# Optimization experiments

Measured on AMD Instinct MI355X. Metric: run time of the kernel, lower is better.

## Reference

```python
import jax, jax.numpy as jnp
import numpy as np
import math

B, T, D, H = 4, 1024, 1024, 16
DK = D // H
TAU_THRESH = 0.3


def setup_inputs() -> dict:
    key = jax.random.key(0)
    ks = jax.random.split(key, 13)
    s = 1.0 / math.sqrt(D)
    return {
        "x": jax.random.normal(ks[0], (B, T, D), dtype=jnp.float32),
        "Wq": jax.random.normal(ks[1], (D, D), dtype=jnp.float32) * s,
        "bq": jax.random.normal(ks[2], (D,), dtype=jnp.float32) * s,
        "Wk": jax.random.normal(ks[3], (D, D), dtype=jnp.float32) * s,
        "bk": jax.random.normal(ks[4], (D,), dtype=jnp.float32) * s,
        "Wv": jax.random.normal(ks[5], (D, D), dtype=jnp.float32) * s,
        "bv": jax.random.normal(ks[6], (D,), dtype=jnp.float32) * s,
        "Wo": jax.random.normal(ks[7], (D, D), dtype=jnp.float32) * s,
        "bo": jax.random.normal(ks[8], (D,), dtype=jnp.float32) * s,
        "Wg1": jax.random.normal(ks[9], (1, D), dtype=jnp.float32) * s,
        "bg1": jax.random.normal(ks[10], (1,), dtype=jnp.float32) * s,
        "Wg2": jax.random.normal(ks[11], (1, D), dtype=jnp.float32) * s,
        "bg2": jax.random.normal(ks[12], (1,), dtype=jnp.float32) * s,
    }


def reference(x, Wq, bq, Wk, bk, Wv, bv, Wo, bo, Wg1, bg1, Wg2, bg2):
    b, t, d = x.shape
    # projections (torch Linear: y = x @ W.T + b)
    Q = (x @ Wq.T + bq).reshape(b, t, H, DK).transpose(0, 2, 1, 3)  # [B,H,T,dk]
    K = (x @ Wk.T + bk).reshape(b, t, H, DK).transpose(0, 2, 1, 3)
    V = (x @ Wv.T + bv).reshape(b, t, H, DK).transpose(0, 2, 1, 3)
    scores = jnp.einsum("bhqd,bhkd->bhqk", Q, K) / math.sqrt(DK)  # [B,H,T,T]
    # confidence gates from first-token query context [B, H*dk] = [B, D]
    context = Q[:, :, 0, :].reshape(b, d)
    q1 = jax.nn.sigmoid(context @ Wg1.T + bg1)  # [B,1]
    q2 = jax.nn.sigmoid(context @ Wg2.T + bg2)  # [B,1]
    c = jnp.clip(q1 * q2, 1e-8, 1.0)            # [B,1]
    tau = jnp.where(c < TAU_THRESH, 1.0 / c, jnp.ones_like(c)).reshape(b, 1, 1, 1)
    p = jax.nn.softmax(scores / tau, axis=-1)
    cb = c.reshape(b, 1, 1, 1)
    p_gated = cb * p + (1.0 - cb) * (1.0 / t)
    u = jnp.mean(1.0 - c, axis=-1, keepdims=True)  # [B,1]
    attn_out = jnp.einsum("bhqk,bhkd->bhqd", p_gated, V)
    attn_out = attn_out.transpose(0, 2, 1, 3).reshape(b, t, d)
    output = attn_out @ Wo.T + bo
    return output, u
```

## Files before the change

kernel.cpp:

```cpp
#include <hip/hip_runtime.h>
#include <stdint.h>

typedef short bf16x8 __attribute__((ext_vector_type(8)));
typedef float f32x4 __attribute__((ext_vector_type(4)));

#define MFMA_BF16(a, b, c) __builtin_amdgcn_mfma_f32_16x16x32_bf16((a), (b), (c), 0, 0, 0)

__device__ __forceinline__ short f2bf(float x) {
  union { float f; uint32_t u; } v; v.f = x;
  uint32_t r = (v.u + 0x7FFFu + ((v.u >> 16) & 1u)) >> 16;
  return (short)r;
}
__device__ __forceinline__ uint32_t rnd_bf_hi(float x) {
  union { float f; uint32_t u; } v; v.f = x;
  return v.u + 0x7FFFu + ((v.u >> 16) & 1u);
}
__device__ __forceinline__ uint32_t pack2bf(float a, float b) {
  return __builtin_amdgcn_perm(rnd_bf_hi(b), rnd_bf_hi(a), 0x07060302);
}
__device__ __forceinline__ float bfbits2f(uint32_t b16) {
  union { uint32_t u; float f; } v; v.u = b16 << 16; return v.f;
}
__device__ __forceinline__ float fexp2(float x) {
#if __has_builtin(__builtin_amdgcn_exp2f)
  return __builtin_amdgcn_exp2f(x);
#else
  return __expf(x * 0.6931471805599453f);
#endif
}
__device__ __forceinline__ void async16(const void* g, void* l) {
  __builtin_amdgcn_global_load_lds(
      (const __attribute__((address_space(1))) uint32_t*)g,
      (__attribute__((address_space(3))) uint32_t*)l, 16, 0, 0);
}

__global__ __launch_bounds__(256) void prep_k(
    const float* __restrict__ x, const float* __restrict__ Wq,
    const float* __restrict__ Wk, const float* __restrict__ Wv,
    const float* __restrict__ Wo, const float* __restrict__ bq,
    short* __restrict__ xb, short* __restrict__ Wqb, short* __restrict__ Wkb,
    short* __restrict__ Wvb, short* __restrict__ Wob, float* __restrict__ ctx) {
  __shared__ float xs[1024];
  const int bid = blockIdx.x;
  const int tid = threadIdx.x;
  if (bid < 8192) {
    const float* src; short* dst; int idx;
    if (bid < 4096) {
      src = x; dst = xb; idx = (bid << 8) + tid;
    } else {
      const int r = bid - 4096;
      const int z = r >> 10;
      src = (z == 0) ? Wq : (z == 1) ? Wk : (z == 2) ? Wv : Wo;
      dst = (z == 0) ? Wqb : (z == 1) ? Wkb : (z == 2) ? Wvb : Wob;
      idx = ((r & 1023) << 8) + tid;
    }
    float4 v = ((const float4*)src)[idx];
    short4 o;
    o.x = f2bf(v.x); o.y = f2bf(v.y); o.z = f2bf(v.z); o.w = f2bf(v.w);
    ((short4*)dst)[idx] = o;
  } else {
    const int r = bid - 8192;
    const int b = r >> 4;
    const int n0 = (r & 15) << 6;
    for (int i = tid; i < 1024; i += 256) xs[i] = x[b * 1048576 + i];
    __syncthreads();
    const int w = tid >> 6, lane = tid & 63;
    const float4* xv4 = (const float4*)xs;
    for (int rr = 0; rr < 16; ++rr) {
      const int n = n0 + (w << 4) + rr;
      const float4* wrow = (const float4*)(Wq + n * 1024);
      float p = 0.f;
#pragma unroll
      for (int c2 = 0; c2 < 4; ++c2) {
        float4 wv = wrow[lane + (c2 << 6)];
        float4 xv = xv4[lane + (c2 << 6)];
        p += xv.x * wv.x + xv.y * wv.y + xv.z * wv.z + xv.w * wv.w;
      }
#pragma unroll
      for (int off = 32; off; off >>= 1) p += __shfl_xor(p, off);
      if (lane == 0) ctx[b * 1024 + n] = p + bq[n];
    }
  }
}

__global__ __launch_bounds__(256) void gates_fin(const float* __restrict__ ctx,
                                                 const float* __restrict__ Wg1,
                                                 const float* __restrict__ bg1,
                                                 const float* __restrict__ Wg2,
                                                 const float* __restrict__ bg2,
                                                 float* __restrict__ gates,
                                                 float* __restrict__ u_out) {
  __shared__ float red[16];
  const int tid = threadIdx.x, w = tid >> 6, lane = tid & 63;
  for (int b = 0; b < 4; ++b) {
    float4 cv = ((const float4*)(ctx + b * 1024))[tid];
    float4 w1 = ((const float4*)Wg1)[tid];
    float4 w2 = ((const float4*)Wg2)[tid];
    float p1 = cv.x * w1.x + cv.y * w1.y + cv.z * w1.z + cv.w * w1.w;
    float p2 = cv.x * w2.x + cv.y * w2.y + cv.z * w2.z + cv.w * w2.w;
#pragma unroll
    for (int off = 32; off; off >>= 1) { p1 += __shfl_xor(p1, off); p2 += __shfl_xor(p2, off); }
    if (lane == 0) { red[w] = p1; red[8 + w] = p2; }
    __syncthreads();
    if (tid == 0) {
      float g1 = red[0] + red[1] + red[2] + red[3] + bg1[0];
      float g2 = red[8] + red[9] + red[10] + red[11] + bg2[0];
      float q1 = 1.f / (1.f + expf(-g1));
      float q2 = 1.f / (1.f + expf(-g2));
      float c = fminf(fmaxf(q1 * q2, 1e-8f), 1.0f);
      gates[b * 2 + 0] = c;
      gates[b * 2 + 1] = (c < 0.3f ? c : 1.0f) * 0.125f * 1.4426950408889634f;
      u_out[b] = 1.0f - c;
    }
    __syncthreads();
  }
}

template <bool SWP>
__device__ __forceinline__ void qkv_core128(
    const short* __restrict__ A, const short* __restrict__ W,
    const float* __restrict__ bias, short* __restrict__ out,
    short* As, short* Bs, int m0, int n0) {
  const int tid = threadIdx.x;
  const int w = tid >> 6, lane = tid & 63;
  const int m15 = lane & 15, quad = lane >> 4;
  const int wr = w >> 1, wc = w & 1;

  f32x4 acc[4][4];
#pragma unroll
  for (int i = 0; i < 4; ++i)
#pragma unroll
    for (int j = 0; j < 4; ++j) { f32x4 zz = {0.f, 0.f, 0.f, 0.f}; acc[i][j] = zz; }

  const int srow = (w << 5) + (lane >> 2);
  const int sxor = (srow >> 1) & 3;
  const int scol = (((lane & 3) ^ sxor) << 3);
  const short* ga0 = A + (m0 + srow) * 1024 + scol;
  const short* ga1 = ga0 + 16 * 1024;
  const short* gb0 = W + (n0 + srow) * 1024 + scol;
  const short* gb1 = gb0 + 16 * 1024;
  short* la0 = &As[srow * 32 + ((lane & 3) << 3)];
  short* la1 = la0 + 512;
  short* lb0 = &Bs[srow * 32 + ((lane & 3) << 3)];
  short* lb1 = lb0 + 512;

  for (int kt = 0; kt < 32; ++kt) {
    async16(ga0, la0); async16(ga1, la1);
    async16(gb0, lb0); async16(gb1, lb1);
    ga0 += 32; ga1 += 32; gb0 += 32; gb1 += 32;
    __syncthreads();
    bf16x8 a[4], b[4];
#pragma unroll
    for (int i = 0; i < 4; ++i) {
      const int ra = (wr << 6) + (i << 4) + m15;
      a[i] = *(const bf16x8*)(&As[ra * 32 + ((quad ^ ((ra >> 1) & 3)) << 3)]);
    }
#pragma unroll
    for (int j = 0; j < 4; ++j) {
      const int rb = (wc << 6) + (j << 4) + m15;
      b[j] = *(const bf16x8*)(&Bs[rb * 32 + ((quad ^ ((rb >> 1) & 3)) << 3)]);
    }
#pragma unroll
    for (int i = 0; i < 4; ++i)
#pragma unroll
      for (int j = 0; j < 4; ++j) {
        if (SWP) acc[i][j] = MFMA_BF16(b[j], a[i], acc[i][j]);
        else     acc[i][j] = MFMA_BF16(a[i], b[j], acc[i][j]);
      }
    __syncthreads();
  }

  if (SWP) {
#pragma unroll
    for (int j = 0; j < 4; ++j) {
      const int n = n0 + (wc << 6) + (j << 4) + (quad << 2);
      const float4 bv = *(const float4*)(bias + n);
      const int hh = n >> 6, dk0 = n & 63;
#pragma unroll
      for (int i = 0; i < 4; ++i) {
        const int m = m0 + (wr << 6) + (i << 4) + m15;
        const int bb = m >> 10, tt = m & 1023;
        uint2 st;
        st.x = pack2bf(acc[i][j][0] + bv.x, acc[i][j][1] + bv.y);
        st.y = pack2bf(acc[i][j][2] + bv.z, acc[i][j][3] + bv.w);
        *(uint2*)(out + (((bb << 4) + hh) << 16) + (tt << 6) + dk0) = st;
      }
    }
  } else {
#pragma unroll
    for (int j = 0; j < 4; ++j) {
      const int n = n0 + (wc << 6) + (j << 4) + m15;
      const float bv = bias[n];
      const int hh = n >> 6, dk = n & 63;
#pragma unroll
      for (int i = 0; i < 4; ++i) {
        const int m = m0 + (wr << 6) + (i << 4) + (quad << 2);
        const int bb = m >> 10, t0 = m & 1023;
        uint2 st;
        st.x = pack2bf(acc[i][j][0] + bv, acc[i][j][1] + bv);
        st.y = pack2bf(acc[i][j][2] + bv, acc[i][j][3] + bv);
        *(uint2*)(out + (((bb << 4) + hh) << 16) + (dk << 10) + t0) = st;
      }
    }
  }
}

__global__ __launch_bounds__(256) void gemm_qkv(
    const short* __restrict__ xb,
    const short* __restrict__ Wqb, const short* __restrict__ Wkb, const short* __restrict__ Wvb,
    const float* __restrict__ bq, const float* __restrict__ bk, const float* __restrict__ bv,
    short* __restrict__ Qh, short* __restrict__ Kh, short* __restrict__ Vt) {
  __shared__ short As[4096];
  __shared__ short Bs[4096];
  const int z = blockIdx.z;
  const int m0 = blockIdx.x << 7, n0 = blockIdx.y << 7;
  if (z == 0)      qkv_core128<true >(xb, Wqb, bq, Qh, As, Bs, m0, n0);
  else if (z == 1) qkv_core128<true >(xb, Wkb, bk, Kh, As, Bs, m0, n0);
  else             qkv_core128<false>(xb, Wvb, bv, Vt, As, Bs, m0, n0);
}

__global__ __launch_bounds__(256) void gemm_out(const short* __restrict__ Ab,
                                                const short* __restrict__ Wo,
                                                const float* __restrict__ bo,
                                                float* __restrict__ Cout) {
  const int m0 = blockIdx.x << 7;
  const int n0 = blockIdx.y << 7;
  const int tid = threadIdx.x;
  const int w = tid >> 6, lane = tid & 63;
  const int m15 = lane & 15, quad = lane >> 4;
  const int wr = w >> 1, wc = w & 1;

  __shared__ short As[4096];
  __shared__ short Bs[4096];

  f32x4 acc[4][4];
#pragma unroll
  for (int i = 0; i < 4; ++i)
#pragma unroll
    for (int j = 0; j < 4; ++j) { f32x4 zz = {0.f, 0.f, 0.f, 0.f}; acc[i][j] = zz; }

  const int srow = (w << 5) + (lane >> 2);
  const int sxor = (srow >> 1) & 3;
  const int scol = (((lane & 3) ^ sxor) << 3);
  const short* ga0 = Ab + (m0 + srow) * 1024 + scol;
  const short* ga1 = ga0 + 16 * 1024;
  const short* gb0 = Wo + (n0 + srow) * 1024 + scol;
  const short* gb1 = gb0 + 16 * 1024;
  short* la0 = &As[srow * 32 + ((lane & 3) << 3)];
  short* la1 = la0 + 512;
  short* lb0 = &Bs[srow * 32 + ((lane & 3) << 3)];
  short* lb1 = lb0 + 512;

  for (int kt = 0; kt < 32; ++kt) {
    async16(ga0, la0); async16(ga1, la1);
    async16(gb0, lb0); async16(gb1, lb1);
    ga0 += 32; ga1 += 32; gb0 += 32; gb1 += 32;
    __syncthreads();
    bf16x8 a[4], b[4];
#pragma unroll
    for (int i = 0; i < 4; ++i) {
      const int ra = (wr << 6) + (i << 4) + m15;
      a[i] = *(const bf16x8*)(&As[ra * 32 + ((quad ^ ((ra >> 1) & 3)) << 3)]);
    }
#pragma unroll
    for (int j = 0; j < 4; ++j) {
      const int rb = (wc << 6) + (j << 4) + m15;
      b[j] = *(const bf16x8*)(&Bs[rb * 32 + ((quad ^ ((rb >> 1) & 3)) << 3)]);
    }
#pragma unroll
    for (int i = 0; i < 4; ++i)
#pragma unroll
      for (int j = 0; j < 4; ++j)
        acc[i][j] = MFMA_BF16(a[i], b[j], acc[i][j]);
    __syncthreads();
  }

#pragma unroll
  for (int j = 0; j < 4; ++j) {
    const int n = n0 + (wc << 6) + (j << 4) + m15;
    const float bb_ = bo[n];
#pragma unroll
    for (int i = 0; i < 4; ++i) {
      const int mb = m0 + (wr << 6) + (i << 4) + (quad << 2);
#pragma unroll
      for (int r = 0; r < 4; ++r)
        Cout[(mb + r) * 1024 + n] = acc[i][j][r] + bb_;
    }
  }
}

__global__ __launch_bounds__(256, 2) void attn_k(const short* __restrict__ Qh,
                                                 const short* __restrict__ Kh,
                                                 const short* __restrict__ Vt,
                                                 const float* __restrict__ gates,
                                                 short* __restrict__ attnb) {
  const int bh = blockIdx.x;
  const int b = bh >> 4, h = bh & 15;
  const int q0 = blockIdx.y << 7;
  const int tid = threadIdx.x;
  const int w = tid >> 6, lane = tid & 63;
  const int m15 = lane & 15, quad = lane >> 4;

  __shared__ short Ks[2][4096];
  __shared__ short Vs[3][4096];

  const short* ksrc = Kh + bh * 65536;
  const short* vsrc = Vt + bh * 65536;

  const float sl = gates[b * 2 + 1];

  const short* qsrcA = Qh + ((bh << 10) + q0 + (w << 4) + m15) * 64;
  const short* qsrcB = qsrcA + 64 * 64;
  const bf16x8 qA0 = *(const bf16x8*)(qsrcA + (quad << 3));
  const bf16x8 qA1 = *(const bf16x8*)(qsrcA + 32 + (quad << 3));
  const bf16x8 qB0 = *(const bf16x8*)(qsrcB + (quad << 3));
  const bf16x8 qB1 = *(const bf16x8*)(qsrcB + 32 + (quad << 3));

  const bf16x8 vone = {0x3F80, 0x3F80, 0x3F80, 0x3F80, 0x3F80, 0x3F80, 0x3F80, 0x3F80};

  const int off0 = tid, off1 = tid + 256;
  const int r0 = off0 >> 3, cb0 = (off0 & 7) ^ (r0 & 7);
  const int r1 = off1 >> 3, cb1 = (off1 & 7) ^ (r1 & 7);

#define STAGE(kv, kb, vb)                                                      \
  do {                                                                         \
    async16(ksrc + (((kv) << 6) + r0) * 64 + (cb0 << 3), &Ks[kb][off0 << 3]);  \
    async16(ksrc + (((kv) << 6) + r1) * 64 + (cb1 << 3), &Ks[kb][off1 << 3]);  \
    async16(vsrc + r0 * 1024 + ((kv) << 6) + (cb0 << 3), &Vs[vb][off0 << 3]);  \
    async16(vsrc + r1 * 1024 + ((kv) << 6) + (cb1 << 3), &Vs[vb][off1 << 3]);  \
  } while (0)

  STAGE(0, 0, 0);

  float lsumA = 0.f, lsumB = 0.f;
  f32x4 oA[4], oB[4], o_mv[4];
#pragma unroll
  for (int jd = 0; jd < 4; ++jd) {
    f32x4 zz = {0.f, 0.f, 0.f, 0.f};
    oA[jd] = zz; oB[jd] = zz; o_mv[jd] = zz;
  }

  const int srcA = ((quad & 1) << 5) + m15;
  const int srcB = srcA + 16;
  const bool selhi = (quad & 2) != 0;

#define BUILD_PF(pf, pk)                                                       \
  do {                                                                         \
    _Pragma("unroll")                                                          \
    for (int Hh = 0; Hh < 2; ++Hh) {                                           \
      uint32_t f[4];                                                           \
      _Pragma("unroll")                                                        \
      for (int rp = 0; rp < 2; ++rp) {                                         \
        uint32_t alo = (uint32_t)__shfl((int)pk[2 * Hh][rp], srcA);            \
        uint32_t ahi = (uint32_t)__shfl((int)pk[2 * Hh + 1][rp], srcA);        \
        uint32_t blo = (uint32_t)__shfl((int)pk[2 * Hh][rp], srcB);            \
        uint32_t bhi = (uint32_t)__shfl((int)pk[2 * Hh + 1][rp], srcB);        \
        f[rp]     = selhi ? ahi : alo;                                         \
        f[2 + rp] = selhi ? bhi : blo;                                         \
      }                                                                        \
      pf[Hh] = *(bf16x8*)f;                                                    \
    }                                                                          \
  } while (0)

#define PV_STEP(Vb, pfa, pfb)                                                  \
  do {                                                                         \
    _Pragma("unroll")                                                          \
    for (int jd = 0; jd < 4; ++jd) {                                           \
      const int row = (jd << 4) + m15;                                         \
      const int sw = row & 7;                                                  \
      bf16x8 v0 = *(const bf16x8*)((Vb) + (row << 6) + ((quad ^ sw) << 3));    \
      bf16x8 v1 = *(const bf16x8*)((Vb) + (row << 6) + (((quad + 4) ^ sw) << 3)); \
      oA[jd] = MFMA_BF16(v0, pfa[0], oA[jd]);                                  \
      oA[jd] = MFMA_BF16(v1, pfa[1], oA[jd]);                                  \
      oB[jd] = MFMA_BF16(v0, pfb[0], oB[jd]);                                  \
      oB[jd] = MFMA_BF16(v1, pfb[1], oB[jd]);                                  \
      o_mv[jd] = MFMA_BF16(v0, vone, o_mv[jd]);                                \
      o_mv[jd] = MFMA_BF16(v1, vone, o_mv[jd]);                                \
    }                                                                          \
  } while (0)

  bf16x8 pfpA[2], pfpB[2];
  pfpA[0] = (bf16x8){0,0,0,0,0,0,0,0}; pfpA[1] = pfpA[0];
  pfpB[0] = pfpA[0]; pfpB[1] = pfpA[0];

  for (int kv = 0; kv < 16; ++kv) {
    __syncthreads();
    if (kv < 15) STAGE(kv + 1, (kv + 1) & 1, (kv + 1) % 3);
    const short* Kb = &Ks[kv & 1][0];

    f32x4 sA[4], sB[4];
#pragma unroll
    for (int s = 0; s < 4; ++s) {
      const int row = (s << 4) + m15;
      const int sw = row & 7;
      bf16x8 a0 = *(const bf16x8*)(Kb + (row << 6) + ((quad ^ sw) << 3));
      bf16x8 a1 = *(const bf16x8*)(Kb + (row << 6) + (((quad + 4) ^ sw) << 3));
      f32x4 zA = {0.f, 0.f, 0.f, 0.f};
      zA = MFMA_BF16(a0, qA0, zA);
      zA = MFMA_BF16(a1, qA1, zA);
      sA[s] = zA;
      f32x4 zB = {0.f, 0.f, 0.f, 0.f};
      zB = MFMA_BF16(a0, qB0, zB);
      zB = MFMA_BF16(a1, qB1, zB);
      sB[s] = zB;
    }

    if (kv > 0) {
      const short* Vb = &Vs[(kv - 1) % 3][0];
      PV_STEP(Vb, pfpA, pfpB);
    }

    uint32_t pkA[4][2], pkB[4][2];
#pragma unroll
    for (int s = 0; s < 4; ++s) {
      float a0 = fexp2(sA[s][0] * sl);
      float a1 = fexp2(sA[s][1] * sl);
      float a2 = fexp2(sA[s][2] * sl);
      float a3 = fexp2(sA[s][3] * sl);
      lsumA += (a0 + a1) + (a2 + a3);
      pkA[s][0] = pack2bf(a0, a1);
      pkA[s][1] = pack2bf(a2, a3);
      float b0 = fexp2(sB[s][0] * sl);
      float b1 = fexp2(sB[s][1] * sl);
      float b2 = fexp2(sB[s][2] * sl);
      float b3 = fexp2(sB[s][3] * sl);
      lsumB += (b0 + b1) + (b2 + b3);
      pkB[s][0] = pack2bf(b0, b1);
      pkB[s][1] = pack2bf(b2, b3);
    }

    bf16x8 pfA[2], pfB[2];
    BUILD_PF(pfA, pkA);
    BUILD_PF(pfB, pkB);
    pfpA[0] = pfA[0]; pfpA[1] = pfA[1];
    pfpB[0] = pfB[0]; pfpB[1] = pfB[1];
  }

  {
    const short* Vb = &Vs[15 % 3][0];
    PV_STEP(Vb, pfpA, pfpB);
  }
#undef STAGE
#undef BUILD_PF
#undef PV_STEP

  float lA = lsumA;
  lA += __shfl_xor(lA, 16);
  lA += __shfl_xor(lA, 32);
  float lB = lsumB;
  lB += __shfl_xor(lB, 16);
  lB += __shfl_xor(lB, 32);

  const float cg = gates[b * 2 + 0];
  const float sc0A = cg / lA;
  const float sc0B = cg / lB;
  const float coef = (1.0f - cg) * (1.0f / 1024.0f);
  const int qrowA = q0 + (w << 4) + m15;
  short* orowA = attnb + ((b << 10) + qrowA) * 1024 + (h << 6);
  short* orowB = orowA + 64 * 1024;
#pragma unroll
  for (int jd = 0; jd < 4; ++jd) {
    uint2 stA;
    stA.x = pack2bf(sc0A * oA[jd][0] + coef * o_mv[jd][0],
                    sc0A * oA[jd][1] + coef * o_mv[jd][1]);
    stA.y = pack2bf(sc0A * oA[jd][2] + coef * o_mv[jd][2],
                    sc0A * oA[jd][3] + coef * o_mv[jd][3]);
    *(uint2*)(orowA + (jd << 4) + (quad << 2)) = stA;
    uint2 stB;
    stB.x = pack2bf(sc0B * oB[jd][0] + coef * o_mv[jd][0],
                    sc0B * oB[jd][1] + coef * o_mv[jd][1]);
    stB.y = pack2bf(sc0B * oB[jd][2] + coef * o_mv[jd][2],
                    sc0B * oB[jd][3] + coef * o_mv[jd][3]);
    *(uint2*)(orowB + (jd << 4) + (quad << 2)) = stB;
  }
}

extern "C" void kernel_launch(void* const* d_in, const int* in_sizes, int n_in,
                              void* d_out, int out_size, void* d_ws, size_t ws_size,
                              hipStream_t stream) {
  const float* x   = (const float*)d_in[0];
  const float* Wq  = (const float*)d_in[1];
  const float* bq  = (const float*)d_in[2];
  const float* Wk  = (const float*)d_in[3];
  const float* bk  = (const float*)d_in[4];
  const float* Wv  = (const float*)d_in[5];
  const float* bv  = (const float*)d_in[6];
  const float* Wo  = (const float*)d_in[7];
  const float* bo  = (const float*)d_in[8];
  const float* Wg1 = (const float*)d_in[9];
  const float* bg1 = (const float*)d_in[10];
  const float* Wg2 = (const float*)d_in[11];
  const float* bg2 = (const float*)d_in[12];
  float* out = (float*)d_out;

  char* ws = (char*)d_ws;
  short* xb   = (short*)(ws + 0);
  short* Wqb  = (short*)(ws + 8388608);
  short* Wkb  = (short*)(ws + 10485760);
  short* Wvb  = (short*)(ws + 12582912);
  short* Wob  = (short*)(ws + 14680064);
  short* Qh   = (short*)(ws + 16777216);
  short* Kh   = (short*)(ws + 25165824);
  short* Vt   = (short*)(ws + 33554432);
  short* attb = (short*)(ws + 41943040);
  float* ctx  = (float*)(ws + 50331648);
  float* gat  = (float*)(ws + 50348032);

  prep_k<<<8256, 256, 0, stream>>>(x, Wq, Wk, Wv, Wo, bq,
                                   xb, Wqb, Wkb, Wvb, Wob, ctx);
  gates_fin<<<1, 256, 0, stream>>>(ctx, Wg1, bg1, Wg2, bg2, gat, out + 4194304);

  gemm_qkv<<<dim3(32, 8, 3), 256, 0, stream>>>(xb, Wqb, Wkb, Wvb, bq, bk, bv,
                                               Qh, Kh, Vt);
  attn_k<<<dim3(64, 8), 256, 0, stream>>>(Qh, Kh, Vt, gat, attb);
  gemm_out<<<dim3(32, 8), 256, 0, stream>>>(attb, Wob, bo, out);
}
```

Measured before the change: 215.0 us.

## Double-buffer LDS tiles in QKV and output projection GEMMs

Both projection GEMM kernels now keep two LDS buffers per operand. The async global-to-LDS load for the next K tile is issued before computing on the current one, and the loop uses one barrier per iteration instead of two. The goal is to hide global load latency behind the MFMA work. In exchange, LDS use per block doubles to 32 KB, which may lower occupancy. Correctness depends on the async copies having finished by the time the single barrier is reached.

```diff
diff --git a/kernel.cpp b/kernel.cpp
--- a/kernel.cpp
+++ b/kernel.cpp
@@ -144,21 +144,30 @@
   short* lb0 = &Bs[srow * 32 + ((lane & 3) << 3)];
   short* lb1 = lb0 + 512;
 
+  async16(ga0, la0); async16(ga1, la1);
+  async16(gb0, lb0); async16(gb1, lb1);
+  __syncthreads();
+
   for (int kt = 0; kt < 32; ++kt) {
-    async16(ga0, la0); async16(ga1, la1);
-    async16(gb0, lb0); async16(gb1, lb1);
-    ga0 += 32; ga1 += 32; gb0 += 32; gb1 += 32;
-    __syncthreads();
+    const int buf = kt & 1;
+    if (kt < 31) {
+      const int nb = (buf ^ 1) << 12;
+      const int off = (kt + 1) << 5;
+      async16(ga0 + off, la0 + nb); async16(ga1 + off, la1 + nb);
+      async16(gb0 + off, lb0 + nb); async16(gb1 + off, lb1 + nb);
+    }
+    const short* Ab = As + (buf << 12);
+    const short* Bb = Bs + (buf << 12);
     bf16x8 a[4], b[4];
 #pragma unroll
     for (int i = 0; i < 4; ++i) {
       const int ra = (wr << 6) + (i << 4) + m15;
-      a[i] = *(const bf16x8*)(&As[ra * 32 + ((quad ^ ((ra >> 1) & 3)) << 3)]);
+      a[i] = *(const bf16x8*)(&Ab[ra * 32 + ((quad ^ ((ra >> 1) & 3)) << 3)]);
     }
 #pragma unroll
     for (int j = 0; j < 4; ++j) {
       const int rb = (wc << 6) + (j << 4) + m15;
-      b[j] = *(const bf16x8*)(&Bs[rb * 32 + ((quad ^ ((rb >> 1) & 3)) << 3)]);
+      b[j] = *(const bf16x8*)(&Bb[rb * 32 + ((quad ^ ((rb >> 1) & 3)) << 3)]);
     }
 #pragma unroll
     for (int i = 0; i < 4; ++i)
@@ -167,7 +176,7 @@
         if (SWP) acc[i][j] = MFMA_BF16(b[j], a[i], acc[i][j]);
         else     acc[i][j] = MFMA_BF16(a[i], b[j], acc[i][j]);
       }
-    __syncthreads();
+    if (kt < 31) __syncthreads();
   }
 
   if (SWP) {
@@ -210,8 +219,8 @@
     const short* __restrict__ Wqb, const short* __restrict__ Wkb, const short* __restrict__ Wvb,
     const float* __restrict__ bq, const float* __restrict__ bk, const float* __restrict__ bv,
     short* __restrict__ Qh, short* __restrict__ Kh, short* __restrict__ Vt) {
-  __shared__ short As[4096];
-  __shared__ short Bs[4096];
+  __shared__ short As[8192];
+  __shared__ short Bs[8192];
   const int z = blockIdx.z;
   const int m0 = blockIdx.x << 7, n0 = blockIdx.y << 7;
   if (z == 0)      qkv_core128<true >(xb, Wqb, bq, Qh, As, Bs, m0, n0);
@@ -219,7 +228,7 @@
   else             qkv_core128<false>(xb, Wvb, bv, Vt, As, Bs, m0, n0);
 }
 
-__global__ __launch_bounds__(256) void gemm_out(const short* __restrict__ Ab,
+__global__ __launch_bounds__(256) void gemm_out(const short* __restrict__ Ab_,
                                                 const short* __restrict__ Wo,
                                                 const float* __restrict__ bo,
                                                 float* __restrict__ Cout) {
@@ -230,8 +239,8 @@
   const int m15 = lane & 15, quad = lane >> 4;
   const int wr = w >> 1, wc = w & 1;
 
-  __shared__ short As[4096];
-  __shared__ short Bs[4096];
+  __shared__ short As[8192];
+  __shared__ short Bs[8192];
 
   f32x4 acc[4][4];
 #pragma unroll
@@ -242,7 +251,7 @@
   const int srow = (w << 5) + (lane >> 2);
   const int sxor = (srow >> 1) & 3;
   const int scol = (((lane & 3) ^ sxor) << 3);
-  const short* ga0 = Ab + (m0 + srow) * 1024 + scol;
+  const short* ga0 = Ab_ + (m0 + srow) * 1024 + scol;
   const short* ga1 = ga0 + 16 * 1024;
   const short* gb0 = Wo + (n0 + srow) * 1024 + scol;
   const short* gb1 = gb0 + 16 * 1024;
@@ -251,28 +260,37 @@
   short* lb0 = &Bs[srow * 32 + ((lane & 3) << 3)];
   short* lb1 = lb0 + 512;
 
+  async16(ga0, la0); async16(ga1, la1);
+  async16(gb0, lb0); async16(gb1, lb1);
+  __syncthreads();
+
   for (int kt = 0; kt < 32; ++kt) {
-    async16(ga0, la0); async16(ga1, la1);
-    async16(gb0, lb0); async16(gb1, lb1);
-    ga0 += 32; ga1 += 32; gb0 += 32; gb1 += 32;
-    __syncthreads();
+    const int buf = kt & 1;
+    if (kt < 31) {
+      const int nb = (buf ^ 1) << 12;
+      const int off = (kt + 1) << 5;
+      async16(ga0 + off, la0 + nb); async16(ga1 + off, la1 + nb);
+      async16(gb0 + off, lb0 + nb); async16(gb1 + off, lb1 + nb);
+    }
+    const short* Ab = As + (buf << 12);
+    const short* Bb = Bs + (buf << 12);
     bf16x8 a[4], b[4];
 #pragma unroll
     for (int i = 0; i < 4; ++i) {
       const int ra = (wr << 6) + (i << 4) + m15;
-      a[i] = *(const bf16x8*)(&As[ra * 32 + ((quad ^ ((ra >> 1) & 3)) << 3)]);
+      a[i] = *(const bf16x8*)(&Ab[ra * 32 + ((quad ^ ((ra >> 1) & 3)) << 3)]);
     }
 #pragma unroll
     for (int j = 0; j < 4; ++j) {
       const int rb = (wc << 6) + (j << 4) + m15;
-      b[j] = *(const bf16x8*)(&Bs[rb * 32 + ((quad ^ ((rb >> 1) & 3)) << 3)]);
+      b[j] = *(const bf16x8*)(&Bb[rb * 32 + ((quad ^ ((rb >> 1) & 3)) << 3)]);
     }
 #pragma unroll
     for (int i = 0; i < 4; ++i)
 #pragma unroll
       for (int j = 0; j < 4; ++j)
         acc[i][j] = MFMA_BF16(a[i], b[j], acc[i][j]);
-    __syncthreads();
+    if (kt < 31) __syncthreads();
   }
 
 #pragma unroll
```

Measured after the change: 215.9 us. Within noise of the previous version (+0.4%).
